# Performance work log

Measured on AMD Instinct MI355X. Metric: run time of the kernel, lower is better.

Reference implementation:

```python
import jax, jax.numpy as jnp
import numpy as np
from jax import lax

B, C, COUT, H, W, DIL = 8, 64, 64, 256, 256, 12
BN_EPS = 1e-5


def conv2d(x, w, dilation, padding):
    # x: [B,Cin,H,W], w: [Cout,Cin,kh,kw]
    return lax.conv_general_dilated(
        x, w, window_strides=(1, 1),
        padding=((padding, padding), (padding, padding)),
        rhs_dilation=(dilation, dilation),
        dimension_numbers=('NCHW', 'OIHW', 'NCHW'))


def grid_sample_bilinear_border(img, sx, sy):
    # img: [B,C,H,W]; sx, sy: [B,H,W] normalized coords in ~[-1,1]
    b, c, h, w = img.shape
    # align_corners=True mapping, border padding == clamp coordinate
    ix = jnp.clip((sx + 1.0) * (w - 1) * 0.5, 0.0, w - 1.0)
    iy = jnp.clip((sy + 1.0) * (h - 1) * 0.5, 0.0, h - 1.0)
    x0 = jnp.floor(ix)
    y0 = jnp.floor(iy)
    wx = ix - x0  # [B,H,W]
    wy = iy - y0
    x0i = x0.astype(jnp.int32)
    y0i = y0.astype(jnp.int32)
    x1i = jnp.minimum(x0i + 1, w - 1)
    y1i = jnp.minimum(y0i + 1, h - 1)

    flat = img.reshape(b, c, h * w)

    def gather(yi, xi):
        idx = (yi * w + xi).reshape(b, 1, h * w)  # broadcast over channels
        return jnp.take_along_axis(flat, idx, axis=2).reshape(b, c, h, w)

    v00 = gather(y0i, x0i)
    v01 = gather(y0i, x1i)
    v10 = gather(y1i, x0i)
    v11 = gather(y1i, x1i)
    wx = wx[:, None]  # [B,1,H,W]
    wy = wy[:, None]
    top = v00 * (1.0 - wx) + v01 * wx
    bot = v10 * (1.0 - wx) + v11 * wx
    return top * (1.0 - wy) + bot * wy


def setup_inputs() -> dict:
    key = jax.random.key(0)
    ks = jax.random.split(key, 6)
    return {
        'x': jax.random.normal(ks[0], (B, C, H, W), jnp.float32),
        'offset_w': jax.random.normal(ks[1], (2, C, 3, 3), jnp.float32) * 0.05,
        'offset_b': jnp.zeros((2,), jnp.float32),
        'conv_w': jax.random.normal(ks[2], (COUT, C, 3, 3), jnp.float32) * 0.05,
        'bn_gamma': jnp.ones((COUT,), jnp.float32),
        'bn_beta': jnp.zeros((COUT,), jnp.float32),
        'bn_mean': jax.random.normal(ks[3], (COUT,), jnp.float32) * 0.1,
        'bn_var': jax.random.uniform(ks[4], (COUT,), jnp.float32, 0.5, 1.5),
    }


def reference(x, offset_w, offset_b, conv_w, bn_gamma, bn_beta, bn_mean, bn_var):
    b, c, h, w = x.shape
    # offset head: conv3x3 -> tanh * 2
    offset = conv2d(x, offset_w, 1, 1) + offset_b[None, :, None, None]
    offset = jnp.tanh(offset) * 2.0  # [B,2,H,W]
    # base grid in [-1,1], x varies along W, y along H (align_corners convention)
    gx = jnp.linspace(-1.0, 1.0, w, dtype=x.dtype)  # [W]
    gy = jnp.linspace(-1.0, 1.0, h, dtype=x.dtype)  # [H]
    sx = gx[None, None, :] + offset[:, 0] / max(float(w - 1), 1.0) * 2.0  # [B,H,W]
    sy = gy[None, :, None] + offset[:, 1] / max(float(h - 1), 1.0) * 2.0
    warped = grid_sample_bilinear_border(x, sx, sy)
    # atrous conv + BN(eval) + ReLU
    y = conv2d(warped, conv_w, DIL, DIL)
    inv = bn_gamma / jnp.sqrt(bn_var + BN_EPS)
    y = y * inv[None, :, None, None] + (bn_beta - bn_mean * inv)[None, :, None, None]
    return jax.nn.relu(y)
```

## Files before the change

### kernel.cpp

```cpp
#include <hip/hip_runtime.h>
#include <hip/hip_bf16.h>
#include <cstdint>

#define HW 256
#define CH 64

typedef __attribute__((ext_vector_type(8))) short bf16x8;
typedef __attribute__((ext_vector_type(4))) float f32x4;

__device__ __forceinline__ float b2f(unsigned short u) {
    union { unsigned int i; float f; } c; c.i = ((unsigned int)u) << 16; return c.f;
}

__device__ __forceinline__ void gload16(const void* g, void* l) {
    __builtin_amdgcn_global_load_lds(
        (const __attribute__((address_space(1))) void*)g,
        (__attribute__((address_space(3))) void*)l, 16, 0, 0);
}

__global__ void wt_kernel(const float* __restrict__ cw, unsigned short* __restrict__ wt) {
    int i = blockIdx.x * 256 + threadIdx.x;
    if (i >= 9 * 64 * 64) return;
    int e = i & 7, j = (i >> 3) & 7, co = (i >> 6) & 63, t9 = i >> 12;
    int ky = t9 / 3, kx = t9 - ky * 3;
    int ci = j * 8 + e;
    float v = cw[co * 576 + ci * 9 + ky * 3 + kx];
    __hip_bfloat16 h = __float2bfloat16(v);
    wt[t9 * 4096 + co * 64 + ((j ^ (co & 7)) * 8) + e] = *(unsigned short*)&h;
}

__global__ __launch_bounds__(256, 3) void offset_warp_kernel(
    const float* __restrict__ x, const float* __restrict__ ow,
    const float* __restrict__ ob, unsigned short* __restrict__ warped)
{
    __shared__ unsigned short sxb[64 * 400 + 24];

    const int orig = blockIdx.x;
    const int lid = (orig & 7) * 256 + (orig >> 3);
    const int bx = lid & 15, by = (lid >> 4) & 15, b = lid >> 8;

    const int t = threadIdx.x;
    const int tx = t & 15, ty = t >> 4;
    const int x0 = bx * 16, y0 = by * 16;
    const int px = x0 + tx, py = y0 + ty;
    const float* xb = x + (size_t)b * CH * HW * HW;

    unsigned int* S32 = (unsigned int*)sxb;
    for (int i = t; i < 12800; i += 256) {
        int c2 = i % 10;
        int r  = i / 10;
        int ly = r % 20;
        int ci = r / 20;
        int gy = y0 + ly - 2;
        int gx = x0 + (c2 << 1) - 2;
        unsigned int pk = 0;
        if ((unsigned)gy < HW && (unsigned)gx < HW) {
            float2 v = *(const float2*)&xb[((size_t)ci * HW + gy) * HW + gx];
            __hip_bfloat16 h0 = __float2bfloat16(v.x);
            __hip_bfloat16 h1 = __float2bfloat16(v.y);
            pk = (unsigned int)*(unsigned short*)&h0 |
                 ((unsigned int)*(unsigned short*)&h1 << 16);
        }
        S32[ci * 200 + ly * 10 + c2] = pk;
    }
    __syncthreads();

    const unsigned int* S = (const unsigned int*)sxb;
    const int shc = ((tx + 1) & 1) * 16;
    float acc0 = ob[0], acc1 = ob[1];
    for (int ci = 0; ci < CH; ++ci) {
        const float* w0 = &ow[ci * 9];
        const float* w1 = &ow[(CH + ci) * 9];
        const int base = ci * 200;
        #pragma unroll
        for (int ky = 0; ky < 3; ++ky) {
            int s = (ty + 1 + ky) * 20 + tx + 1;
            int w = base + (s >> 1);
            unsigned long long u =
                ((unsigned long long)S[w + 1] << 32) | (unsigned long long)S[w];
            u >>= shc;
            float t0 = b2f((unsigned short)u);
            float t1 = b2f((unsigned short)(u >> 16));
            float t2 = b2f((unsigned short)(u >> 32));
            acc0 = fmaf(t0, w0[ky * 3 + 0], acc0);
            acc1 = fmaf(t0, w1[ky * 3 + 0], acc1);
            acc0 = fmaf(t1, w0[ky * 3 + 1], acc0);
            acc1 = fmaf(t1, w1[ky * 3 + 1], acc1);
            acc0 = fmaf(t2, w0[ky * 3 + 2], acc0);
            acc1 = fmaf(t2, w1[ky * 3 + 2], acc1);
        }
    }

    float off0 = tanhf(acc0) * 2.0f;
    float off1 = tanhf(acc1) * 2.0f;
    float ix = fminf(fmaxf((float)px + off0, 0.f), 255.f);
    float iy = fminf(fmaxf((float)py + off1, 0.f), 255.f);
    float fx0 = floorf(ix), fy0 = floorf(iy);
    float wx = ix - fx0, wy = iy - fy0;
    int lx0 = (int)fx0 - x0 + 2;
    int ly0 = (int)fy0 - y0 + 2;
    float w00 = (1.f - wx) * (1.f - wy), w01 = wx * (1.f - wy);
    float w10 = (1.f - wx) * wy,         w11 = wx * wy;
    const int offw = ly0 * 20 + lx0;
    const int w0i = offw >> 1;
    const int shg = (offw & 1) * 16;

    unsigned short* wb = warped + ((size_t)b * (HW * HW) + (size_t)py * HW + px) * CH;
    const int key = px & 7;
    #pragma unroll
    for (int j = 0; j < 8; ++j) {
        unsigned int pk[4];
        #pragma unroll
        for (int p = 0; p < 4; ++p) {
            unsigned int pw = 0;
            #pragma unroll
            for (int h = 0; h < 2; ++h) {
                int ci = j * 8 + p * 2 + h;
                int bw = ci * 200 + w0i;
                unsigned long long ra =
                    ((unsigned long long)S[bw + 1] << 32) | (unsigned long long)S[bw];
                ra >>= shg;
                unsigned long long rb =
                    ((unsigned long long)S[bw + 11] << 32) | (unsigned long long)S[bw + 10];
                rb >>= shg;
                float v = b2f((unsigned short)ra) * w00 +
                          b2f((unsigned short)(ra >> 16)) * w01 +
                          b2f((unsigned short)rb) * w10 +
                          b2f((unsigned short)(rb >> 16)) * w11;
                __hip_bfloat16 hh = __float2bfloat16(v);
                pw |= ((unsigned int)*(unsigned short*)&hh) << (16 * h);
            }
            pk[p] = pw;
        }
        uint4 q; q.x = pk[0]; q.y = pk[1]; q.z = pk[2]; q.w = pk[3];
        *(uint4*)&wb[(size_t)((j ^ key) * 8)] = q;
    }
}

__global__ __launch_bounds__(256, 2) void conv_mfma_kernel(
    const unsigned short* __restrict__ warped, const unsigned short* __restrict__ wtb,
    const float* __restrict__ gamma, const float* __restrict__ beta,
    const float* __restrict__ mean, const float* __restrict__ var,
    float* __restrict__ out)
{
    __shared__ __align__(16) unsigned short sa[280 * 64];
    __shared__ __align__(16) unsigned short sw[3 * 64 * 64];
    __shared__ float sinv[64], sbias[64];

    const int t = threadIdx.x;
    const int orig = blockIdx.x;
    const int lid = (orig & 7) * 256 + (orig >> 3);
    const int oy = lid & 255, b = lid >> 8;
    const int wid = t >> 6, lane = t & 63;
    const int l15 = lane & 15, l4 = lane >> 4;

    if (t < 64) {
        float inv = gamma[t] * rsqrtf(var[t] + 1e-5f);
        sinv[t] = inv;
        sbias[t] = beta[t] - mean[t] * inv;
    }
    if (t < 192) {
        int p = t >> 3, sub = t & 7;
        int px = (p < 12) ? p : (256 + p);
        *(uint4*)&sa[px * 64 + sub * 8] = make_uint4(0, 0, 0, 0);
    }

    f32x4 acc[4][4];
    #pragma unroll
    for (int m = 0; m < 4; ++m)
        #pragma unroll
        for (int n = 0; n < 4; ++n) acc[m][n] = (f32x4){0.f, 0.f, 0.f, 0.f};

    const size_t bbase = (size_t)b * (HW * (size_t)HW * CH);

    for (int ky = 0; ky < 3; ++ky) {
        __syncthreads();
        int gy = oy + (ky - 1) * 12;
        if (gy >= 0 && gy < HW) {
            const char* src = (const char*)(warped + bbase + (size_t)gy * (HW * CH));
            #pragma unroll
            for (int r = 0; r < 8; ++r)
                gload16(src + r * 4096 + t * 16,
                        (char*)sa + 1536 + r * 4096 + wid * 1024);
        } else {
            #pragma unroll
            for (int r = 0; r < 8; ++r)
                *(uint4*)((char*)sa + 1536 + r * 4096 + t * 16) = make_uint4(0, 0, 0, 0);
        }
        {
            const char* wsrc = (const char*)wtb + ky * 24576;
            #pragma unroll
            for (int r = 0; r < 6; ++r)
                gload16(wsrc + r * 4096 + t * 16,
                        (char*)sw + r * 4096 + wid * 1024);
        }
        asm volatile("s_waitcnt vmcnt(0)" ::: "memory");
        __syncthreads();

        #pragma unroll
        for (int kx = 0; kx < 3; ++kx) {
            #pragma unroll
            for (int ks = 0; ks < 2; ++ks) {
                const int jg = ks * 4 + l4;
                bf16x8 af[4], bfr[4];
                #pragma unroll
                for (int m = 0; m < 4; ++m) {
                    int co = m * 16 + l15;
                    int jp = jg ^ (co & 7);
                    af[m] = *(const bf16x8*)&sw[(kx * 64 + co) * 64 + jp * 8];
                }
                #pragma unroll
                for (int n = 0; n < 4; ++n) {
                    int pl = wid * 64 + n * 16 + l15 + kx * 12;
                    int c = jg ^ ((pl + 4) & 7);
                    bfr[n] = *(const bf16x8*)&sa[pl * 64 + c * 8];
                }
                #pragma unroll
                for (int m = 0; m < 4; ++m)
                    #pragma unroll
                    for (int n = 0; n < 4; ++n)
                        acc[m][n] = __builtin_amdgcn_mfma_f32_16x16x32_bf16(
                            af[m], bfr[n], acc[m][n], 0, 0, 0);
            }
        }
    }

    #pragma unroll
    for (int m = 0; m < 4; ++m) {
        #pragma unroll
        for (int r = 0; r < 4; ++r) {
            int co = m * 16 + l4 * 4 + r;
            float inv = sinv[co], bs = sbias[co];
            float* orow = out + (((size_t)b * CH + co) * HW + oy) * HW + wid * 64 + l15;
            #pragma unroll
            for (int n = 0; n < 4; ++n)
                orow[n * 16] = fmaxf(fmaf(acc[m][n][r], inv, bs), 0.f);
        }
    }
}

extern "C" void kernel_launch(void* const* d_in, const int* in_sizes, int n_in,
                              void* d_out, int out_size, void* d_ws, size_t ws_size,
                              hipStream_t stream) {
    const float* x     = (const float*)d_in[0];
    const float* ow    = (const float*)d_in[1];
    const float* ob    = (const float*)d_in[2];
    const float* cw    = (const float*)d_in[3];
    const float* gamma = (const float*)d_in[4];
    const float* beta  = (const float*)d_in[5];
    const float* mean  = (const float*)d_in[6];
    const float* var   = (const float*)d_in[7];
    float* out = (float*)d_out;

    unsigned short* warped = (unsigned short*)d_ws;
    unsigned short* wtb    = (unsigned short*)((char*)d_ws + (size_t)8 * CH * HW * HW * 2);

    wt_kernel<<<(9 * 64 * 64 + 255) / 256, 256, 0, stream>>>(cw, wtb);

    offset_warp_kernel<<<dim3(2048), 256, 0, stream>>>(x, ow, ob, warped);

    conv_mfma_kernel<<<dim3(2048), 256, 0, stream>>>(warped, wtb, gamma, beta, mean, var, out);
}
```

Before: 201.8 us.

## Double-buffer fp32 halo staging per 8-channel group and gather warp taps from global

The offset-head kernel now stages the input halo in fp32, 8 channels at a time, into a two-slot shared buffer. Interior tiles use async global-to-LDS loads so the next group's load overlaps compute on the current one. This shrinks shared memory enough to raise the occupancy hint from 3 to 5 blocks. The bilinear warp now reads its four taps directly from global fp32 memory instead of the bf16 shared tile, which also drops the bf16 rounding on the sampled inputs. The cost is many scattered global loads (256 per pixel), which depend on cache hits.

Measured after the change: 459.0 us. +127.4%, slower.

```diff
diff --git a/kernel.cpp b/kernel.cpp
--- a/kernel.cpp
+++ b/kernel.cpp
@@ -29,65 +29,92 @@
     wt[t9 * 4096 + co * 64 + ((j ^ (co & 7)) * 8) + e] = *(unsigned short*)&h;
 }
 
-__global__ __launch_bounds__(256, 3) void offset_warp_kernel(
+__global__ __launch_bounds__(256, 5) void offset_warp_kernel(
     const float* __restrict__ x, const float* __restrict__ ow,
     const float* __restrict__ ob, unsigned short* __restrict__ warped)
 {
-    __shared__ unsigned short sxb[64 * 400 + 24];
+    __shared__ __align__(16) float sg[2][3328];
 
     const int orig = blockIdx.x;
     const int lid = (orig & 7) * 256 + (orig >> 3);
     const int bx = lid & 15, by = (lid >> 4) & 15, b = lid >> 8;
-
     const int t = threadIdx.x;
     const int tx = t & 15, ty = t >> 4;
+    const int wid = t >> 6;
     const int x0 = bx * 16, y0 = by * 16;
     const int px = x0 + tx, py = y0 + ty;
     const float* xb = x + (size_t)b * CH * HW * HW;
-
-    unsigned int* S32 = (unsigned int*)sxb;
-    for (int i = t; i < 12800; i += 256) {
-        int c2 = i % 10;
-        int r  = i / 10;
-        int ly = r % 20;
-        int ci = r / 20;
-        int gy = y0 + ly - 2;
-        int gx = x0 + (c2 << 1) - 2;
-        unsigned int pk = 0;
-        if ((unsigned)gy < HW && (unsigned)gx < HW) {
-            float2 v = *(const float2*)&xb[((size_t)ci * HW + gy) * HW + gx];
-            __hip_bfloat16 h0 = __float2bfloat16(v.x);
-            __hip_bfloat16 h1 = __float2bfloat16(v.y);
-            pk = (unsigned int)*(unsigned short*)&h0 |
-                 ((unsigned int)*(unsigned short*)&h1 << 16);
-        }
-        S32[ci * 200 + ly * 10 + c2] = pk;
-    }
+    const bool interior = (bx > 0) && (bx < 15) && (by > 0) && (by < 15);
+
+    auto stage = [&](int g) {
+        float* buf = sg[g & 1];
+        if (interior) {
+            const float* base = xb + (size_t)(g * 8) * (HW * HW) + (y0 - 2) * HW + (x0 - 2);
+            #pragma unroll
+            for (int k = 0; k < 4; ++k) {
+                if (k < 3 || wid == 0) {
+                    int c = k * 256 + t;
+                    int ci8 = c / 100;
+                    int rem = c - ci8 * 100;
+                    int ly = rem / 5;
+                    int c4 = rem - ly * 5;
+                    const float* ga = (c < 800)
+                        ? (base + ci8 * (HW * HW) + ly * HW + c4 * 4)
+                        : xb;
+                    gload16(ga, (char*)buf + k * 4096 + wid * 1024);
+                }
+            }
+        } else {
+            for (int k = 0; k < 13; ++k) {
+                int i = k * 256 + t;
+                if (i < 3200) {
+                    int ci8 = i / 400;
+                    int rem = i - ci8 * 400;
+                    int ly = rem / 20;
+                    int lx = rem - ly * 20;
+                    int gy = y0 + ly - 2, gx = x0 + lx - 2;
+                    float v = 0.f;
+                    if ((unsigned)gy < HW && (unsigned)gx < HW)
+                        v = xb[(size_t)(g * 8 + ci8) * (HW * HW) + gy * HW + gx];
+                    buf[i] = v;
+                }
+            }
+        }
+    };
+
+    stage(0);
+    asm volatile("s_waitcnt vmcnt(0)" ::: "memory");
     __syncthreads();
 
-    const unsigned int* S = (const unsigned int*)sxb;
-    const int shc = ((tx + 1) & 1) * 16;
     float acc0 = ob[0], acc1 = ob[1];
-    for (int ci = 0; ci < CH; ++ci) {
-        const float* w0 = &ow[ci * 9];
-        const float* w1 = &ow[(CH + ci) * 9];
-        const int base = ci * 200;
-        #pragma unroll
-        for (int ky = 0; ky < 3; ++ky) {
-            int s = (ty + 1 + ky) * 20 + tx + 1;
-            int w = base + (s >> 1);
-            unsigned long long u =
-                ((unsigned long long)S[w + 1] << 32) | (unsigned long long)S[w];
-            u >>= shc;
-            float t0 = b2f((unsigned short)u);
-            float t1 = b2f((unsigned short)(u >> 16));
-            float t2 = b2f((unsigned short)(u >> 32));
-            acc0 = fmaf(t0, w0[ky * 3 + 0], acc0);
-            acc1 = fmaf(t0, w1[ky * 3 + 0], acc1);
-            acc0 = fmaf(t1, w0[ky * 3 + 1], acc0);
-            acc1 = fmaf(t1, w1[ky * 3 + 1], acc1);
-            acc0 = fmaf(t2, w0[ky * 3 + 2], acc0);
-            acc1 = fmaf(t2, w1[ky * 3 + 2], acc1);
+    const int par = (tx + 1) & 1;
+    for (int g = 0; g < 8; ++g) {
+        if (g < 7) stage(g + 1);
+        const float* buf = sg[g & 1];
+        #pragma unroll
+        for (int ci8 = 0; ci8 < 8; ++ci8) {
+            const int ci = g * 8 + ci8;
+            const float* w0 = &ow[ci * 9];
+            const float* w1 = &ow[(CH + ci) * 9];
+            const float* q0 = buf + ci8 * 400 + (ty + 1) * 20 + ((tx + 1) & ~1);
+            #pragma unroll
+            for (int ky = 0; ky < 3; ++ky) {
+                const float2 qa = *(const float2*)(q0 + ky * 20);
+                const float2 qb = *(const float2*)(q0 + ky * 20 + 2);
+                float t0 = par ? qa.y : qa.x;
+                float t1 = par ? qb.x : qa.y;
+                float t2 = par ? qb.y : qb.x;
+                acc0 = fmaf(t0, w0[ky * 3 + 0], acc0);
+                acc1 = fmaf(t0, w1[ky * 3 + 0], acc1);
+                acc0 = fmaf(t1, w0[ky * 3 + 1], acc0);
+                acc1 = fmaf(t1, w1[ky * 3 + 1], acc1);
+                acc0 = fmaf(t2, w0[ky * 3 + 2], acc0);
+                acc1 = fmaf(t2, w1[ky * 3 + 2], acc1);
+            }
+        }
+        if (g < 7) {
+            asm volatile("s_waitcnt vmcnt(0)" ::: "memory");
+            __syncthreads();
         }
     }
 
@@ -97,13 +124,13 @@
     float iy = fminf(fmaxf((float)py + off1, 0.f), 255.f);
     float fx0 = floorf(ix), fy0 = floorf(iy);
     float wx = ix - fx0, wy = iy - fy0;
-    int lx0 = (int)fx0 - x0 + 2;
-    int ly0 = (int)fy0 - y0 + 2;
+    int x0i = (int)fx0, y0i = (int)fy0;
+    int x1i = min(x0i + 1, HW - 1), y1i = min(y0i + 1, HW - 1);
     float w00 = (1.f - wx) * (1.f - wy), w01 = wx * (1.f - wy);
     float w10 = (1.f - wx) * wy,         w11 = wx * wy;
-    const int offw = ly0 * 20 + lx0;
-    const int w0i = offw >> 1;
-    const int shg = (offw & 1) * 16;
+
+    const int oA0 = y0i * HW + x0i, oA1 = y0i * HW + x1i;
+    const int oB0 = y1i * HW + x0i, oB1 = y1i * HW + x1i;
 
     unsigned short* wb = warped + ((size_t)b * (HW * HW) + (size_t)py * HW + px) * CH;
     const int key = px & 7;
@@ -116,17 +143,9 @@
             #pragma unroll
             for (int h = 0; h < 2; ++h) {
                 int ci = j * 8 + p * 2 + h;
-                int bw = ci * 200 + w0i;
-                unsigned long long ra =
-                    ((unsigned long long)S[bw + 1] << 32) | (unsigned long long)S[bw];
-                ra >>= shg;
-                unsigned long long rb =
-                    ((unsigned long long)S[bw + 11] << 32) | (unsigned long long)S[bw + 10];
-                rb >>= shg;
-                float v = b2f((unsigned short)ra) * w00 +
-                          b2f((unsigned short)(ra >> 16)) * w01 +
-                          b2f((unsigned short)rb) * w10 +
-                          b2f((unsigned short)(rb >> 16)) * w11;
+                const float* cp = xb + (size_t)ci * (HW * HW);
+                float v = cp[oA0] * w00 + cp[oA1] * w01 +
+                          cp[oB0] * w10 + cp[oB1] * w11;
                 __hip_bfloat16 hh = __float2bfloat16(v);
                 pw |= ((unsigned int)*(unsigned short*)&hh) << (16 * h);
             }
```

## Split offset conv and warp into separate double-buffered kernels

Applied to the files above, without the earlier changes.

Replaces the fused offset+warp kernel with two kernels. The first computes the offset conv in fp32 over 32x32 tiles with 4 outputs per thread, double-buffering channel groups through registers into LDS, and writes offsets to a workspace buffer. The second reads those offsets and the input in double-buffered 8-channel groups to do the bilinear warp. The aim is to overlap global loads with compute and reduce the large LDS footprint of the fused kernel. The cost is reading x twice, plus an extra launch and an offsets round-trip.

Result: slower. 373.2 us (+84.9%).

```diff
diff --git a/kernel.cpp b/kernel.cpp
--- a/kernel.cpp
+++ b/kernel.cpp
@@ -11,7 +11,10 @@
 __device__ __forceinline__ float b2f(unsigned short u) {
     union { unsigned int i; float f; } c; c.i = ((unsigned int)u) << 16; return c.f;
 }
-
+__device__ __forceinline__ unsigned short f2b(float f) {
+    __hip_bfloat16 h = __float2bfloat16(f);
+    return *(unsigned short*)&h;
+}
 __device__ __forceinline__ void gload16(const void* g, void* l) {
     __builtin_amdgcn_global_load_lds(
         (const __attribute__((address_space(1))) void*)g,
@@ -24,117 +27,196 @@
     int e = i & 7, j = (i >> 3) & 7, co = (i >> 6) & 63, t9 = i >> 12;
     int ky = t9 / 3, kx = t9 - ky * 3;
     int ci = j * 8 + e;
-    float v = cw[co * 576 + ci * 9 + ky * 3 + kx];
-    __hip_bfloat16 h = __float2bfloat16(v);
-    wt[t9 * 4096 + co * 64 + ((j ^ (co & 7)) * 8) + e] = *(unsigned short*)&h;
-}
-
-__global__ __launch_bounds__(256, 3) void offset_warp_kernel(
+    wt[t9 * 4096 + co * 64 + ((j ^ (co & 7)) * 8) + e] = f2b(cw[co * 576 + ci * 9 + ky * 3 + kx]);
+}
+
+__global__ __launch_bounds__(256) void offset_conv_kernel(
     const float* __restrict__ x, const float* __restrict__ ow,
-    const float* __restrict__ ob, unsigned short* __restrict__ warped)
+    const float* __restrict__ ob, float* __restrict__ offs)
 {
-    __shared__ unsigned short sxb[64 * 400 + 24];
-
-    const int orig = blockIdx.x;
-    const int lid = (orig & 7) * 256 + (orig >> 3);
+    __shared__ __align__(16) float sg[2][4 * 34 * 40];
+
+    const int lid = blockIdx.x;
+    const int bx = lid & 7, by = (lid >> 3) & 7, b = lid >> 6;
+    const int t = threadIdx.x;
+    const int i = t & 7, r = t >> 3;
+    const int x0 = bx * 32, y0 = by * 32;
+    const float* xb = x + (size_t)b * CH * HW * HW;
+
+    float rv[10][2];
+    auto issue = [&](int g) {
+        #pragma unroll
+        for (int k = 0; k < 10; ++k) {
+            int idx = k * 256 + t;
+            rv[k][0] = 0.f; rv[k][1] = 0.f;
+            if (idx < 2448) {
+                int ci4 = idx / 612;
+                int rem = idx - ci4 * 612;
+                int ly  = rem / 18, k2 = rem - ly * 18;
+                int gy = y0 - 1 + ly, gx = x0 - 2 + 2 * k2;
+                bool ok = ((unsigned)gy < 256u) && ((unsigned)gx < 256u);
+                int cy = min(max(gy, 0), 255), cx = min(max(gx, 0), 254);
+                float2 v = *(const float2*)&xb[((size_t)(g * 4 + ci4) * HW + cy) * HW + cx];
+                if (ok) { rv[k][0] = v.x; rv[k][1] = v.y; }
+            }
+        }
+    };
+    auto commit = [&](float* buf) {
+        #pragma unroll
+        for (int k = 0; k < 10; ++k) {
+            int idx = k * 256 + t;
+            if (idx < 2448) {
+                int ci4 = idx / 612;
+                int rem = idx - ci4 * 612;
+                int ly  = rem / 18, k2 = rem - ly * 18;
+                *(float2*)&buf[ci4 * 1360 + ly * 40 + 2 * k2] = make_float2(rv[k][0], rv[k][1]);
+            }
+        }
+    };
+
+    issue(0); commit(sg[0]);
+    __syncthreads();
+
+    float a0[4], a1[4];
+    #pragma unroll
+    for (int j = 0; j < 4; ++j) { a0[j] = ob[0]; a1[j] = ob[1]; }
+
+    for (int g = 0; g < 16; ++g) {
+        if (g < 15) issue(g + 1);
+        const float* buf = sg[g & 1];
+        #pragma unroll
+        for (int ci4 = 0; ci4 < 4; ++ci4) {
+            int ci = g * 4 + ci4;
+            const float* w0 = &ow[ci * 9];
+            const float* w1 = &ow[(CH + ci) * 9];
+            const float* pb = buf + ci4 * 1360 + 4 * i;
+            #pragma unroll
+            for (int ky = 0; ky < 3; ++ky) {
+                const float4 qa = *(const float4*)(pb + (r + ky) * 40);
+                const float4 qb = *(const float4*)(pb + (r + ky) * 40 + 4);
+                float tv[8] = {qa.x, qa.y, qa.z, qa.w, qb.x, qb.y, qb.z, qb.w};
+                #pragma unroll
+                for (int kx = 0; kx < 3; ++kx) {
+                    float wa = w0[ky * 3 + kx], wbv = w1[ky * 3 + kx];
+                    #pragma unroll
+                    for (int j = 0; j < 4; ++j) {
+                        a0[j] = fmaf(tv[j + kx + 1], wa, a0[j]);
+                        a1[j] = fmaf(tv[j + kx + 1], wbv, a1[j]);
+                    }
+                }
+            }
+        }
+        if (g < 15) { commit(sg[(g + 1) & 1]); __syncthreads(); }
+    }
+
+    const int py = y0 + r, px0 = x0 + 4 * i;
+    float o[8];
+    #pragma unroll
+    for (int j = 0; j < 4; ++j) {
+        o[2 * j]     = tanhf(a0[j]) * 2.0f;
+        o[2 * j + 1] = tanhf(a1[j]) * 2.0f;
+    }
+    float* op = offs + (((size_t)b * HW + py) * HW + px0) * 2;
+    *(float4*)op       = make_float4(o[0], o[1], o[2], o[3]);
+    *(float4*)(op + 4) = make_float4(o[4], o[5], o[6], o[7]);
+}
+
+__global__ __launch_bounds__(256, 4) void warp_kernel(
+    const float* __restrict__ x, const float* __restrict__ offs,
+    unsigned short* __restrict__ warped)
+{
+    __shared__ __align__(16) unsigned int sx[2][8 * 20 * 11];
+
+    const int lid = blockIdx.x;
     const int bx = lid & 15, by = (lid >> 4) & 15, b = lid >> 8;
-
     const int t = threadIdx.x;
     const int tx = t & 15, ty = t >> 4;
     const int x0 = bx * 16, y0 = by * 16;
     const int px = x0 + tx, py = y0 + ty;
     const float* xb = x + (size_t)b * CH * HW * HW;
 
-    unsigned int* S32 = (unsigned int*)sxb;
-    for (int i = t; i < 12800; i += 256) {
-        int c2 = i % 10;
-        int r  = i / 10;
-        int ly = r % 20;
-        int ci = r / 20;
-        int gy = y0 + ly - 2;
-        int gx = x0 + (c2 << 1) - 2;
-        unsigned int pk = 0;
-        if ((unsigned)gy < HW && (unsigned)gx < HW) {
-            float2 v = *(const float2*)&xb[((size_t)ci * HW + gy) * HW + gx];
-            __hip_bfloat16 h0 = __float2bfloat16(v.x);
-            __hip_bfloat16 h1 = __float2bfloat16(v.y);
-            pk = (unsigned int)*(unsigned short*)&h0 |
-                 ((unsigned int)*(unsigned short*)&h1 << 16);
-        }
-        S32[ci * 200 + ly * 10 + c2] = pk;
-    }
-    __syncthreads();
-
-    const unsigned int* S = (const unsigned int*)sxb;
-    const int shc = ((tx + 1) & 1) * 16;
-    float acc0 = ob[0], acc1 = ob[1];
-    for (int ci = 0; ci < CH; ++ci) {
-        const float* w0 = &ow[ci * 9];
-        const float* w1 = &ow[(CH + ci) * 9];
-        const int base = ci * 200;
-        #pragma unroll
-        for (int ky = 0; ky < 3; ++ky) {
-            int s = (ty + 1 + ky) * 20 + tx + 1;
-            int w = base + (s >> 1);
-            unsigned long long u =
-                ((unsigned long long)S[w + 1] << 32) | (unsigned long long)S[w];
-            u >>= shc;
-            float t0 = b2f((unsigned short)u);
-            float t1 = b2f((unsigned short)(u >> 16));
-            float t2 = b2f((unsigned short)(u >> 32));
-            acc0 = fmaf(t0, w0[ky * 3 + 0], acc0);
-            acc1 = fmaf(t0, w1[ky * 3 + 0], acc1);
-            acc0 = fmaf(t1, w0[ky * 3 + 1], acc0);
-            acc1 = fmaf(t1, w1[ky * 3 + 1], acc1);
-            acc0 = fmaf(t2, w0[ky * 3 + 2], acc0);
-            acc1 = fmaf(t2, w1[ky * 3 + 2], acc1);
-        }
-    }
-
-    float off0 = tanhf(acc0) * 2.0f;
-    float off1 = tanhf(acc1) * 2.0f;
-    float ix = fminf(fmaxf((float)px + off0, 0.f), 255.f);
-    float iy = fminf(fmaxf((float)py + off1, 0.f), 255.f);
+    float rv[7][2];
+    auto issue = [&](int g) {
+        #pragma unroll
+        for (int k = 0; k < 7; ++k) {
+            int idx = k * 256 + t;
+            rv[k][0] = 0.f; rv[k][1] = 0.f;
+            if (idx < 1600) {
+                int ci8 = idx / 200;
+                int rem = idx - ci8 * 200;
+                int ly = rem / 10, k2 = rem - ly * 10;
+                int gy = y0 - 2 + ly, gx = x0 - 2 + 2 * k2;
+                bool ok = ((unsigned)gy < 256u) && ((unsigned)gx < 256u);
+                int cy = min(max(gy, 0), 255), cx = min(max(gx, 0), 254);
+                float2 v = *(const float2*)&xb[((size_t)(g * 8 + ci8) * HW + cy) * HW + cx];
+                if (ok) { rv[k][0] = v.x; rv[k][1] = v.y; }
+            }
+        }
+    };
+    auto commit = [&](unsigned int* buf) {
+        #pragma unroll
+        for (int k = 0; k < 7; ++k) {
+            int idx = k * 256 + t;
+            if (idx < 1600) {
+                int ci8 = idx / 200;
+                int rem = idx - ci8 * 200;
+                int ly = rem / 10, k2 = rem - ly * 10;
+                buf[ci8 * 220 + ly * 11 + k2] =
+                    (unsigned int)f2b(rv[k][0]) | ((unsigned int)f2b(rv[k][1]) << 16);
+            }
+        }
+    };
+
+    const float2 off = *(const float2*)&offs[(((size_t)b * HW + py) * HW + px) * 2];
+    float ix = fminf(fmaxf((float)px + off.x, 0.f), 255.f);
+    float iy = fminf(fmaxf((float)py + off.y, 0.f), 255.f);
     float fx0 = floorf(ix), fy0 = floorf(iy);
     float wx = ix - fx0, wy = iy - fy0;
     int lx0 = (int)fx0 - x0 + 2;
     int ly0 = (int)fy0 - y0 + 2;
     float w00 = (1.f - wx) * (1.f - wy), w01 = wx * (1.f - wy);
     float w10 = (1.f - wx) * wy,         w11 = wx * wy;
-    const int offw = ly0 * 20 + lx0;
-    const int w0i = offw >> 1;
-    const int shg = (offw & 1) * 16;
-
-    unsigned short* wb = warped + ((size_t)b * (HW * HW) + (size_t)py * HW + px) * CH;
-    const int key = px & 7;
-    #pragma unroll
-    for (int j = 0; j < 8; ++j) {
-        unsigned int pk[4];
+    const int wbase = ly0 * 11 + (lx0 >> 1);
+    const int sh = (lx0 & 1) * 16;
+
+    issue(0); commit(sx[0]);
+    __syncthreads();
+
+    uint4 pk[8];
+    #pragma unroll
+    for (int g = 0; g < 8; ++g) {
+        if (g < 7) issue(g + 1);
+        const unsigned int* S = sx[g & 1];
+        unsigned int res[4];
         #pragma unroll
         for (int p = 0; p < 4; ++p) {
             unsigned int pw = 0;
             #pragma unroll
             for (int h = 0; h < 2; ++h) {
-                int ci = j * 8 + p * 2 + h;
-                int bw = ci * 200 + w0i;
+                int base = (p * 2 + h) * 220 + wbase;
                 unsigned long long ra =
-                    ((unsigned long long)S[bw + 1] << 32) | (unsigned long long)S[bw];
-                ra >>= shg;
+                    ((unsigned long long)S[base + 1] << 32) | (unsigned long long)S[base];
+                ra >>= sh;
                 unsigned long long rb =
-                    ((unsigned long long)S[bw + 11] << 32) | (unsigned long long)S[bw + 10];
-                rb >>= shg;
+                    ((unsigned long long)S[base + 12] << 32) | (unsigned long long)S[base + 11];
+                rb >>= sh;
                 float v = b2f((unsigned short)ra) * w00 +
                           b2f((unsigned short)(ra >> 16)) * w01 +
                           b2f((unsigned short)rb) * w10 +
                           b2f((unsigned short)(rb >> 16)) * w11;
-                __hip_bfloat16 hh = __float2bfloat16(v);
-                pw |= ((unsigned int)*(unsigned short*)&hh) << (16 * h);
-            }
-            pk[p] = pw;
-        }
-        uint4 q; q.x = pk[0]; q.y = pk[1]; q.z = pk[2]; q.w = pk[3];
-        *(uint4*)&wb[(size_t)((j ^ key) * 8)] = q;
-    }
+                pw |= ((unsigned int)f2b(v)) << (16 * h);
+            }
+            res[p] = pw;
+        }
+        pk[g] = make_uint4(res[0], res[1], res[2], res[3]);
+        if (g < 7) { commit(sx[(g + 1) & 1]); __syncthreads(); }
+    }
+
+    unsigned short* wbp = warped + ((size_t)b * (HW * HW) + (size_t)py * HW + px) * CH;
+    const int key = px & 7;
+    #pragma unroll
+    for (int g = 0; g < 8; ++g)
+        *(uint4*)&wbp[(size_t)((g ^ key) * 8)] = pk[g];
 }
 
 __global__ __launch_bounds__(256, 2) void conv_mfma_kernel(
@@ -253,11 +335,14 @@
     float* out = (float*)d_out;
 
     unsigned short* warped = (unsigned short*)d_ws;
-    unsigned short* wtb    = (unsigned short*)((char*)d_ws + (size_t)8 * CH * HW * HW * 2);
+    unsigned short* wtb    = (unsigned short*)((char*)d_ws + 67108864);
+    float*          offsb  = (float*)((char*)d_ws + 67108864 + 73728);
 
     wt_kernel<<<(9 * 64 * 64 + 255) / 256, 256, 0, stream>>>(cw, wtb);
 
-    offset_warp_kernel<<<dim3(2048), 256, 0, stream>>>(x, ow, ob, warped);
+    offset_conv_kernel<<<dim3(512), 256, 0, stream>>>(x, ow, ob, offsb);
+
+    warp_kernel<<<dim3(2048), 256, 0, stream>>>(x, offsb, warped);
 
     conv_mfma_kernel<<<dim3(2048), 256, 0, stream>>>(warped, wtb, gamma, beta, mean, var, out);
 }
```
